# Performance work log

Measured on AMD Instinct MI355X. Metric: run time of the kernel, lower is better.

The kernel has to match this reference:

```python
import jax, jax.numpy as jnp
import numpy as np

B, T, E, H = 4, 2048, 1024, 16
HD = E // H  # head_dim = 64


def setup_inputs() -> dict:
    key = jax.random.key(0)
    ks = jax.random.split(key, 6)
    s_in = 1.0 / np.sqrt(HD)
    s_e = 1.0 / np.sqrt(E)
    return {
        "x": jax.random.normal(ks[0], (B, T, E), dtype=jnp.float32),
        # per-head qkv linear: weight [H, HD, 3*HD], bias [H, 3*HD]
        "W_qkv": jax.random.uniform(ks[1], (H, HD, 3 * HD), dtype=jnp.float32, minval=-s_in, maxval=s_in),
        "b_qkv": jax.random.uniform(ks[2], (H, 3 * HD), dtype=jnp.float32, minval=-s_in, maxval=s_in),
        # output projection [E, E]
        "W_proj": jax.random.uniform(ks[3], (E, E), dtype=jnp.float32, minval=-s_e, maxval=s_e),
        "b_proj": jax.random.uniform(ks[4], (E,), dtype=jnp.float32, minval=-s_e, maxval=s_e),
    }


def reference(x, W_qkv, b_qkv, W_proj, b_proj):
    b, t, e = x.shape
    h, hd = W_qkv.shape[0], W_qkv.shape[1]
    # Each head consumes its own contiguous slice of the channel dim.
    xh = x.reshape(b, t, h, hd)  # [B,T,H,HD]
    qkv = jnp.einsum("bthd,hde->bthe", xh, W_qkv) + b_qkv  # [B,T,H,3*HD]
    q, k, v = jnp.split(qkv, 3, axis=-1)  # each [B,T,H,HD]
    scale = 1.0 / (hd ** 0.5 + 1e-05)  # matches (embed_dim ** 0.5 + 1e-05) with embed_dim=head_dim
    attn = jnp.einsum("bthd,bshd->bhts", q, k) * scale  # [B,H,T,T]
    causal = jnp.tril(jnp.ones((t, t), dtype=bool))
    attn = jnp.where(causal, attn, -jnp.inf)
    attn = jax.nn.softmax(attn, axis=-1)
    out = jnp.einsum("bhts,bshd->bthd", attn, v).reshape(b, t, e)  # concat heads
    # dropout is identity in eval mode
    return out @ W_proj.T + b_proj
```

## Files before the change

### kernel.cpp

```cpp
#include <hip/hip_runtime.h>
#include <hip/hip_bf16.h>

#define B_ 4
#define T_ 2048
#define E_ 1024
#define H_ 16
#define HD_ 64

typedef __attribute__((ext_vector_type(8))) short bf16x8;
typedef __attribute__((ext_vector_type(4))) float f32x4;
typedef __attribute__((ext_vector_type(16))) float f32x16;

__device__ inline ushort f2b(float f) {
  union { __hip_bfloat16 h; ushort u; } c;
  c.h = __float2bfloat16(f);
  return c.u;
}
__device__ inline short f2bs(float f) {
  union { __hip_bfloat16 h; short s; } c;
  c.h = __float2bfloat16(f);
  return c.s;
}
__device__ inline int cvtpk(float lo, float hi) {
  int r;
  asm("v_cvt_pk_bf16_f32 %0, %1, %2" : "=v"(r) : "v"(lo), "v"(hi));
  return r;
}
__device__ inline f32x16 zero16() {
  f32x16 z;
#pragma unroll
  for (int i = 0; i < 16; ++i) z[i] = 0.0f;
  return z;
}

__device__ inline void gload16(const ushort* gsrc, ushort* lds_uniform_base) {
  __builtin_amdgcn_global_load_lds(
      (const __attribute__((address_space(1))) void*)gsrc,
      (__attribute__((address_space(3))) void*)lds_uniform_base, 16, 0, 0);
}

__global__ __launch_bounds__(256) void cvt_w_kernel(const float* __restrict__ Wq,
                                                    ushort* __restrict__ Wt) {
  int gtid = blockIdx.x * 256 + threadIdx.x;
  int h = gtid / (HD_ * 192);
  int rem = gtid % (HD_ * 192);
  int d = rem / 192;
  int e = rem % 192;
  Wt[h * (192 * HD_) + e * HD_ + d] = f2b(Wq[gtid]);
}

__global__ __launch_bounds__(256) void cvt_wproj_kernel(const float* __restrict__ Wp,
                                                        ushort* __restrict__ Wb) {
  int i = (blockIdx.x * 256 + threadIdx.x) * 4;
  float4 f = *reinterpret_cast<const float4*>(Wp + i);
  ushort4 u;
  u.x = f2b(f.x); u.y = f2b(f.y); u.z = f2b(f.z); u.w = f2b(f.w);
  *reinterpret_cast<ushort4*>(Wb + i) = u;
}

__global__ __launch_bounds__(256) void qkv_kernel(const float* __restrict__ x,
                                                  const ushort* __restrict__ Wt,
                                                  const float* __restrict__ bq,
                                                  ushort* __restrict__ Q,
                                                  ushort* __restrict__ K,
                                                  ushort* __restrict__ Vt) {
  const float SCALE = (1.0f / (8.0f + 1e-5f)) * 1.4426950408889634f;
  int wave = threadIdx.x >> 6, lane = threadIdx.x & 63;
  int lo = lane & 15, hi = lane >> 4;
  int bh = blockIdx.y, b = bh >> 4, h = bh & 15;
  int t0 = blockIdx.x * 64 + wave * 16;

  const float* xr = x + (size_t)(b * T_ + t0 + lo) * E_ + h * HD_;
  bf16x8 af[2];
#pragma unroll
  for (int c = 0; c < 2; ++c) {
    float4 f0 = *reinterpret_cast<const float4*>(xr + c * 32 + hi * 8);
    float4 f1 = *reinterpret_cast<const float4*>(xr + c * 32 + hi * 8 + 4);
    bf16x8 v;
    v[0] = f2bs(f0.x); v[1] = f2bs(f0.y); v[2] = f2bs(f0.z); v[3] = f2bs(f0.w);
    v[4] = f2bs(f1.x); v[5] = f2bs(f1.y); v[6] = f2bs(f1.z); v[7] = f2bs(f1.w);
    af[c] = v;
  }

  const ushort* Wh = Wt + h * (192 * HD_);
#pragma unroll
  for (int nt = 0; nt < 12; ++nt) {
    int n0 = nt * 16;
    bf16x8 bf0 = *reinterpret_cast<const bf16x8*>(Wh + (size_t)(n0 + lo) * HD_ + hi * 8);
    bf16x8 bf1 = *reinterpret_cast<const bf16x8*>(Wh + (size_t)(n0 + lo) * HD_ + 32 + hi * 8);
    f32x4 acc = {0.0f, 0.0f, 0.0f, 0.0f};
    acc = __builtin_amdgcn_mfma_f32_16x16x32_bf16(af[0], bf0, acc, 0, 0, 0);
    acc = __builtin_amdgcn_mfma_f32_16x16x32_bf16(af[1], bf1, acc, 0, 0, 0);

    int which = nt >> 2;
    int hd = (nt & 3) * 16 + lo;
    float bias = bq[h * 192 + n0 + lo];
    if (which < 2) {
      ushort* dst = which == 0 ? Q : K;
      float sc = which == 0 ? SCALE : 1.0f;
#pragma unroll
      for (int r = 0; r < 4; ++r) {
        int t = t0 + hi * 4 + r;
        dst[((size_t)bh * T_ + t) * HD_ + hd] = f2b((acc[r] + bias) * sc);
      }
    } else {
      ushort4 u;
      u.x = f2b(acc[0] + bias);
      u.y = f2b(acc[1] + bias);
      u.z = f2b(acc[2] + bias);
      u.w = f2b(acc[3] + bias);
      int col = t0 + hi * 4 + hd * 8;
      col &= (T_ - 1);
      *reinterpret_cast<ushort4*>(Vt + ((size_t)bh * HD_ + hd) * T_ + col) = u;
    }
  }
}

__global__ __launch_bounds__(256) void attn_kernel(const ushort* __restrict__ Q,
                                                   const ushort* __restrict__ K,
                                                   const ushort* __restrict__ Vt,
                                                   ushort* __restrict__ AO) {
  __shared__ ushort Ks[3][64 * 64];
  __shared__ ushort Vs[3][64 * 64];

  int wave = threadIdx.x >> 6, lane = threadIdx.x & 63;
  int q5 = lane & 31, hi5 = lane >> 5;
  int bh = blockIdx.x, b = bh >> 4, h = bh & 15;
  int qt = (T_ / 128 - 1) - blockIdx.y;
  int qw = qt * 128 + wave * 32;

  const ushort* Kbh = K + (size_t)bh * T_ * HD_;
  const ushort* Vbh = Vt + (size_t)bh * HD_ * T_;

  bf16x8 qf[4];
#pragma unroll
  for (int ks = 0; ks < 4; ++ks)
    qf[ks] = *reinterpret_cast<const bf16x8*>(
        Q + ((size_t)bh * T_ + qw + q5) * HD_ + ks * 16 + hi5 * 8);

  f32x16 ot[2];
  ot[0] = zero16(); ot[1] = zero16();
  float mreg = -1e30f, lreg = 0.0f;

  int srow = lane >> 3;
  int sch = lane & 7;

  int ntiles = qt * 2 + 2;

#define STAGE(BUF, TILE)                                                        \
  {                                                                             \
    int kt_ = (TILE) << 6;                                                      \
    _Pragma("unroll")                                                           \
    for (int rep = 0; rep < 2; ++rep) {                                         \
      int row = rep * 32 + wave * 8 + srow;                                     \
      const ushort* gk = Kbh + (size_t)(kt_ + row) * HD_ + ((sch ^ (row & 7)) * 8); \
      gload16(gk, &Ks[BUF][(rep * 32 + wave * 8) * 64]);                        \
      int col = (kt_ + ((sch ^ (row & 7)) + row) * 8) & (T_ - 1);               \
      const ushort* gv = Vbh + (size_t)row * T_ + col;                          \
      gload16(gv, &Vs[BUF][(rep * 32 + wave * 8) * 64]);                        \
    }                                                                           \
  }

  STAGE(0, 0);
  STAGE(1, 1);

  int cur = 0;
  for (int tile = 0; tile < ntiles; ++tile) {
    int kt = tile << 6;
    asm volatile("s_waitcnt vmcnt(4)" ::: "memory");
    __builtin_amdgcn_s_barrier();
    {
      int pre = (tile + 2 < ntiles) ? tile + 2 : 0;
      int pb = cur + 2; if (pb >= 3) pb -= 3;
      STAGE(pb, pre);
    }

    if (kt <= qw + 31) {
      f32x16 s[2];
#pragma unroll
      for (int g = 0; g < 2; ++g) {
        int krow = g * 32 + q5;
        bf16x8 kf[4];
#pragma unroll
        for (int ks = 0; ks < 4; ++ks)
          kf[ks] = *reinterpret_cast<const bf16x8*>(
              &Ks[cur][krow * 64 + (((2 * ks + hi5) ^ (krow & 7)) * 8)]);
        f32x16 acc = zero16();
        __builtin_amdgcn_s_setprio(1);
#pragma unroll
        for (int ks = 0; ks < 4; ++ks)
          acc = __builtin_amdgcn_mfma_f32_32x32x16_bf16(kf[ks], qf[ks], acc, 0, 0, 0);
        __builtin_amdgcn_s_setprio(0);
        s[g] = acc;
      }
      if (kt + 63 > qw) {
        int q = qw + q5;
#pragma unroll
        for (int g = 0; g < 2; ++g)
#pragma unroll
          for (int r = 0; r < 16; ++r) {
            int key = kt + g * 32 + (r & 3) + 8 * (r >> 2) + 4 * hi5;
            if (key > q) s[g][r] = -1e30f;
          }
      }
      float t8[8];
#pragma unroll
      for (int i = 0; i < 8; ++i)
        t8[i] = fmaxf(fmaxf(s[0][i], s[0][i + 8]), fmaxf(s[1][i], s[1][i + 8]));
      float mx = fmaxf(fmaxf(fmaxf(t8[0], t8[1]), fmaxf(t8[2], t8[3])),
                       fmaxf(fmaxf(t8[4], t8[5]), fmaxf(t8[6], t8[7])));
      mx = fmaxf(mx, __shfl_xor(mx, 32));
      float nm = fmaxf(mreg, mx);
      float alpha = exp2f(mreg - nm);
      mreg = nm;
#pragma unroll
      for (int g = 0; g < 2; ++g)
#pragma unroll
        for (int r = 0; r < 16; ++r)
          s[g][r] = exp2f(s[g][r] - nm);
      float u8[8];
#pragma unroll
      for (int i = 0; i < 8; ++i)
        u8[i] = (s[0][i] + s[0][i + 8]) + (s[1][i] + s[1][i + 8]);
      float rs = ((u8[0] + u8[1]) + (u8[2] + u8[3])) + ((u8[4] + u8[5]) + (u8[6] + u8[7]));
      rs += __shfl_xor(rs, 32);
      lreg = lreg * alpha + rs;
#pragma unroll
      for (int nh = 0; nh < 2; ++nh)
#pragma unroll
        for (int r = 0; r < 16; ++r) ot[nh][r] *= alpha;

      bf16x8 pb4[4];
#pragma unroll
      for (int ks = 0; ks < 4; ++ks) {
        int g = ks >> 1;
        int R0 = 2 * (ks & 1), R1 = R0 + 1;
        int a0w0 = cvtpk(s[g][4 * R0 + 0], s[g][4 * R0 + 1]);
        int a0w1 = cvtpk(s[g][4 * R0 + 2], s[g][4 * R0 + 3]);
        int a1w0 = cvtpk(s[g][4 * R1 + 0], s[g][4 * R1 + 1]);
        int a1w1 = cvtpk(s[g][4 * R1 + 2], s[g][4 * R1 + 3]);
        int pA0w0 = __shfl_xor(a0w0, 32);
        int pA0w1 = __shfl_xor(a0w1, 32);
        int pA1w0 = __shfl_xor(a1w0, 32);
        int pA1w1 = __shfl_xor(a1w1, 32);
        int4 w;
        w.x = hi5 ? pA1w0 : a0w0;
        w.y = hi5 ? pA1w1 : a0w1;
        w.z = hi5 ? a1w0 : pA0w0;
        w.w = hi5 ? a1w1 : pA0w1;
        pb4[ks] = *reinterpret_cast<bf16x8*>(&w);
      }
#pragma unroll
      for (int nh = 0; nh < 2; ++nh) {
        int vrow = nh * 32 + q5;
        bf16x8 vf[4];
#pragma unroll
        for (int ks = 0; ks < 4; ++ks)
          vf[ks] = *reinterpret_cast<const bf16x8*>(
              &Vs[cur][vrow * 64 + (((2 * ks + hi5) ^ (vrow & 7)) * 8)]);
        __builtin_amdgcn_s_setprio(1);
#pragma unroll
        for (int ks = 0; ks < 4; ++ks)
          ot[nh] = __builtin_amdgcn_mfma_f32_32x32x16_bf16(vf[ks], pb4[ks], ot[nh], 0, 0, 0);
        __builtin_amdgcn_s_setprio(0);
      }
    }
    cur = (cur == 2) ? 0 : cur + 1;
  }
#undef STAGE

  float inv = 1.0f / lreg;
  int t = qw + q5;
  ushort* aop = AO + ((size_t)(b * T_ + t) * H_ + h) * HD_;
#pragma unroll
  for (int nh = 0; nh < 2; ++nh)
#pragma unroll
    for (int R = 0; R < 4; ++R) {
      ushort4 u;
      u.x = f2b(ot[nh][4 * R + 0] * inv);
      u.y = f2b(ot[nh][4 * R + 1] * inv);
      u.z = f2b(ot[nh][4 * R + 2] * inv);
      u.w = f2b(ot[nh][4 * R + 3] * inv);
      *reinterpret_cast<ushort4*>(aop + nh * 32 + 8 * R + 4 * hi5) = u;
    }
}

__global__ __launch_bounds__(256) void proj_kernel(const ushort* __restrict__ A,
                                                   const ushort* __restrict__ Wb,
                                                   const float* __restrict__ bias,
                                                   float* __restrict__ out) {
  __shared__ ushort As[2][128 * 32];
  __shared__ ushort Bs[2][128 * 32];
  int tid = threadIdx.x;
  int wave = tid >> 6, lane = tid & 63;
  int lo = lane & 15, hi = lane >> 4;
  int wr = wave >> 1, wc = wave & 1;
  int m0 = blockIdx.y * 128, n0 = blockIdx.x * 128;

  int srow4 = lane >> 2;
  int sch4 = lane & 3;
  int swz = sch4 ^ ((srow4 >> 1) & 3);

#define PSTAGE(BUF, K0)                                                          \
  {                                                                              \
    _Pragma("unroll")                                                            \
    for (int rep = 0; rep < 2; ++rep) {                                          \
      int row = wave * 32 + rep * 16 + srow4;                                    \
      gload16(A + (size_t)(m0 + row) * E_ + (K0) + swz * 8,                      \
              &As[BUF][(wave * 32 + rep * 16) * 32]);                            \
      gload16(Wb + (size_t)(n0 + row) * E_ + (K0) + swz * 8,                     \
              &Bs[BUF][(wave * 32 + rep * 16) * 32]);                            \
    }                                                                            \
  }

  f32x4 acc[4][4] = {};
  PSTAGE(0, 0);
  asm volatile("s_waitcnt vmcnt(0)" ::: "memory");
  __syncthreads();

  int cur = 0;
  for (int k0 = 0; k0 < E_; k0 += 32) {
    int kpre = (k0 + 32) & (E_ - 1);
    PSTAGE(cur ^ 1, kpre);
    bf16x8 af[4], bfr[4];
#pragma unroll
    for (int i = 0; i < 4; ++i) {
      int row = wr * 64 + i * 16 + lo;
      af[i] = *reinterpret_cast<const bf16x8*>(
          &As[cur][row * 32 + ((hi ^ ((row >> 1) & 3)) * 8)]);
    }
#pragma unroll
    for (int j = 0; j < 4; ++j) {
      int row = wc * 64 + j * 16 + lo;
      bfr[j] = *reinterpret_cast<const bf16x8*>(
          &Bs[cur][row * 32 + ((hi ^ ((row >> 1) & 3)) * 8)]);
    }
    __builtin_amdgcn_s_setprio(1);
#pragma unroll
    for (int i = 0; i < 4; ++i)
#pragma unroll
      for (int j = 0; j < 4; ++j)
        acc[i][j] = __builtin_amdgcn_mfma_f32_16x16x32_bf16(af[i], bfr[j], acc[i][j], 0, 0, 0);
    __builtin_amdgcn_s_setprio(0);
    asm volatile("s_waitcnt vmcnt(0)" ::: "memory");
    __syncthreads();
    cur ^= 1;
  }
#undef PSTAGE

#pragma unroll
  for (int i = 0; i < 4; ++i)
#pragma unroll
    for (int r = 0; r < 4; ++r) {
      int mm = m0 + wr * 64 + i * 16 + hi * 4 + r;
      float* orow = out + (size_t)mm * E_ + n0 + wc * 64;
#pragma unroll
      for (int j = 0; j < 4; ++j)
        orow[j * 16 + lo] = acc[i][j][r] + bias[n0 + wc * 64 + j * 16 + lo];
    }
}

extern "C" void kernel_launch(void* const* d_in, const int* in_sizes, int n_in,
                              void* d_out, int out_size, void* d_ws, size_t ws_size,
                              hipStream_t stream) {
  (void)in_sizes; (void)n_in; (void)out_size; (void)ws_size;
  const float* x  = (const float*)d_in[0];
  const float* Wq = (const float*)d_in[1];
  const float* bq = (const float*)d_in[2];
  const float* Wp = (const float*)d_in[3];
  const float* bp = (const float*)d_in[4];
  float* out = (float*)d_out;

  const size_t NQ = (size_t)B_ * H_ * T_ * HD_;
  ushort* ws = (ushort*)d_ws;
  ushort* Q  = ws;
  ushort* K  = ws + NQ;
  ushort* Vt = ws + 2 * NQ;
  ushort* AO = ws + 3 * NQ;
  ushort* Wb = ws + 4 * NQ;
  ushort* Wt = ws + 4 * NQ + (size_t)E_ * E_;

  cvt_w_kernel<<<dim3(768), dim3(256), 0, stream>>>(Wq, Wt);
  cvt_wproj_kernel<<<dim3(1024), dim3(256), 0, stream>>>(Wp, Wb);
  qkv_kernel<<<dim3(T_ / 64, B_ * H_), dim3(256), 0, stream>>>(x, Wt, bq, Q, K, Vt);
  attn_kernel<<<dim3(B_ * H_, 16), dim3(256), 0, stream>>>(Q, K, Vt, AO);
  proj_kernel<<<dim3(E_ / 128, (B_ * T_) / 128), dim3(256), 0, stream>>>(AO, Wb, bp, out);
}
```

Baseline: 153.4 us.

## Process two 32-query groups per wave and stage KV tiles in pairs

The attention kernel now gives each wave 64 queries, split into two 32-row groups that share each K/V fragment read from LDS. The block tile grows to 256 queries and the grid shrinks to 8 blocks per head, ordered by interleaving long and short causal rows. Shared memory goes from three to four buffers, and K/V tiles are prefetched two at a time, waiting on all outstanding loads (vmcnt(0)) before each pair. This doubles the MFMA work per LDS read, but raises register pressure, halves the block count, and coarsens load balancing.

Result: slower. 215.2 us (+40.3%).

```diff
diff --git a/kernel.cpp b/kernel.cpp
--- a/kernel.cpp
+++ b/kernel.cpp
@@ -120,32 +120,37 @@
                                                    const ushort* __restrict__ K,
                                                    const ushort* __restrict__ Vt,
                                                    ushort* __restrict__ AO) {
-  __shared__ ushort Ks[3][64 * 64];
-  __shared__ ushort Vs[3][64 * 64];
+  __shared__ ushort Ks[4][64 * 64];
+  __shared__ ushort Vs[4][64 * 64];
 
   int wave = threadIdx.x >> 6, lane = threadIdx.x & 63;
   int q5 = lane & 31, hi5 = lane >> 5;
   int bh = blockIdx.x, b = bh >> 4, h = bh & 15;
-  int qt = (T_ / 128 - 1) - blockIdx.y;
-  int qw = qt * 128 + wave * 32;
+  int y = blockIdx.y;
+  int qt = (y < 4) ? (7 - y) : (y - 4);
+  int qw = qt * 256 + wave * 64;
 
   const ushort* Kbh = K + (size_t)bh * T_ * HD_;
   const ushort* Vbh = Vt + (size_t)bh * HD_ * T_;
 
-  bf16x8 qf[4];
-#pragma unroll
-  for (int ks = 0; ks < 4; ++ks)
-    qf[ks] = *reinterpret_cast<const bf16x8*>(
+  bf16x8 qfA[4], qfB[4];
+#pragma unroll
+  for (int ks = 0; ks < 4; ++ks) {
+    qfA[ks] = *reinterpret_cast<const bf16x8*>(
         Q + ((size_t)bh * T_ + qw + q5) * HD_ + ks * 16 + hi5 * 8);
-
-  f32x16 ot[2];
-  ot[0] = zero16(); ot[1] = zero16();
-  float mreg = -1e30f, lreg = 0.0f;
+    qfB[ks] = *reinterpret_cast<const bf16x8*>(
+        Q + ((size_t)bh * T_ + qw + 32 + q5) * HD_ + ks * 16 + hi5 * 8);
+  }
+
+  f32x16 otA[2], otB[2];
+  otA[0] = zero16(); otA[1] = zero16();
+  otB[0] = zero16(); otB[1] = zero16();
+  float mA = -1e30f, lA = 0.0f, mB = -1e30f, lB = 0.0f;
 
   int srow = lane >> 3;
   int sch = lane & 7;
 
-  int ntiles = qt * 2 + 2;
+  int ntiles = qt * 4 + 4;
 
 #define STAGE(BUF, TILE)                                                        \
   {                                                                             \
@@ -161,128 +166,154 @@
     }                                                                           \
   }
 
+  auto mask_g = [&](f32x16 (&s)[2], int qwg, int kt) {
+    int q = qwg + q5;
+#pragma unroll
+    for (int g = 0; g < 2; ++g)
+#pragma unroll
+      for (int r = 0; r < 16; ++r) {
+        int key = kt + g * 32 + (r & 3) + 8 * (r >> 2) + 4 * hi5;
+        if (key > q) s[g][r] = -1e30f;
+      }
+  };
+  auto softmax_g = [&](f32x16 (&s)[2], float& mreg, float& lreg, f32x16 (&ot)[2]) {
+    float t8[8];
+#pragma unroll
+    for (int i = 0; i < 8; ++i)
+      t8[i] = fmaxf(fmaxf(s[0][i], s[0][i + 8]), fmaxf(s[1][i], s[1][i + 8]));
+    float mx = fmaxf(fmaxf(fmaxf(t8[0], t8[1]), fmaxf(t8[2], t8[3])),
+                     fmaxf(fmaxf(t8[4], t8[5]), fmaxf(t8[6], t8[7])));
+    mx = fmaxf(mx, __shfl_xor(mx, 32));
+    float nm = fmaxf(mreg, mx);
+    float alpha = exp2f(mreg - nm);
+    mreg = nm;
+#pragma unroll
+    for (int g = 0; g < 2; ++g)
+#pragma unroll
+      for (int r = 0; r < 16; ++r)
+        s[g][r] = exp2f(s[g][r] - nm);
+    float u8[8];
+#pragma unroll
+    for (int i = 0; i < 8; ++i)
+      u8[i] = (s[0][i] + s[0][i + 8]) + (s[1][i] + s[1][i + 8]);
+    float rs = ((u8[0] + u8[1]) + (u8[2] + u8[3])) + ((u8[4] + u8[5]) + (u8[6] + u8[7]));
+    rs += __shfl_xor(rs, 32);
+    lreg = lreg * alpha + rs;
+#pragma unroll
+    for (int nh = 0; nh < 2; ++nh)
+#pragma unroll
+      for (int r = 0; r < 16; ++r) ot[nh][r] *= alpha;
+  };
+  auto repack_g = [&](const f32x16 (&s)[2], bf16x8 (&pb)[4]) {
+#pragma unroll
+    for (int ks = 0; ks < 4; ++ks) {
+      int g = ks >> 1;
+      int R0 = 2 * (ks & 1), R1 = R0 + 1;
+      int a0w0 = cvtpk(s[g][4 * R0 + 0], s[g][4 * R0 + 1]);
+      int a0w1 = cvtpk(s[g][4 * R0 + 2], s[g][4 * R0 + 3]);
+      int a1w0 = cvtpk(s[g][4 * R1 + 0], s[g][4 * R1 + 1]);
+      int a1w1 = cvtpk(s[g][4 * R1 + 2], s[g][4 * R1 + 3]);
+      int pA0w0 = __shfl_xor(a0w0, 32);
+      int pA0w1 = __shfl_xor(a0w1, 32);
+      int pA1w0 = __shfl_xor(a1w0, 32);
+      int pA1w1 = __shfl_xor(a1w1, 32);
+      int4 w;
+      w.x = hi5 ? pA1w0 : a0w0;
+      w.y = hi5 ? pA1w1 : a0w1;
+      w.z = hi5 ? a1w0 : pA0w0;
+      w.w = hi5 ? a1w1 : pA0w1;
+      pb[ks] = *reinterpret_cast<bf16x8*>(&w);
+    }
+  };
+
+  auto compute_tile = [&](int tile, int buf) {
+    int kt = tile << 6;
+    if (kt > qw + 31) return;
+    f32x16 sA[2], sB[2];
+#pragma unroll
+    for (int g = 0; g < 2; ++g) {
+      int krow = g * 32 + q5;
+      bf16x8 kf[4];
+#pragma unroll
+      for (int ks = 0; ks < 4; ++ks)
+        kf[ks] = *reinterpret_cast<const bf16x8*>(
+            &Ks[buf][krow * 64 + (((2 * ks + hi5) ^ (krow & 7)) * 8)]);
+      f32x16 aA = zero16(), aB = zero16();
+      __builtin_amdgcn_s_setprio(1);
+#pragma unroll
+      for (int ks = 0; ks < 4; ++ks)
+        aA = __builtin_amdgcn_mfma_f32_32x32x16_bf16(kf[ks], qfA[ks], aA, 0, 0, 0);
+#pragma unroll
+      for (int ks = 0; ks < 4; ++ks)
+        aB = __builtin_amdgcn_mfma_f32_32x32x16_bf16(kf[ks], qfB[ks], aB, 0, 0, 0);
+      __builtin_amdgcn_s_setprio(0);
+      sA[g] = aA; sB[g] = aB;
+    }
+    if (kt + 63 > qw) {
+      mask_g(sA, qw, kt);
+      mask_g(sB, qw + 32, kt);
+    }
+    softmax_g(sA, mA, lA, otA);
+    softmax_g(sB, mB, lB, otB);
+    bf16x8 pbA[4], pbB[4];
+    repack_g(sA, pbA);
+    repack_g(sB, pbB);
+#pragma unroll
+    for (int nh = 0; nh < 2; ++nh) {
+      int vrow = nh * 32 + q5;
+      bf16x8 vf[4];
+#pragma unroll
+      for (int ks = 0; ks < 4; ++ks)
+        vf[ks] = *reinterpret_cast<const bf16x8*>(
+            &Vs[buf][vrow * 64 + (((2 * ks + hi5) ^ (vrow & 7)) * 8)]);
+      __builtin_amdgcn_s_setprio(1);
+#pragma unroll
+      for (int ks = 0; ks < 4; ++ks)
+        otA[nh] = __builtin_amdgcn_mfma_f32_32x32x16_bf16(vf[ks], pbA[ks], otA[nh], 0, 0, 0);
+#pragma unroll
+      for (int ks = 0; ks < 4; ++ks)
+        otB[nh] = __builtin_amdgcn_mfma_f32_32x32x16_bf16(vf[ks], pbB[ks], otB[nh], 0, 0, 0);
+      __builtin_amdgcn_s_setprio(0);
+    }
+  };
+
   STAGE(0, 0);
   STAGE(1, 1);
 
-  int cur = 0;
-  for (int tile = 0; tile < ntiles; ++tile) {
-    int kt = tile << 6;
-    asm volatile("s_waitcnt vmcnt(4)" ::: "memory");
+  int npairs = ntiles >> 1;
+  for (int p = 0; p < npairs; ++p) {
+    int t0 = 2 * p, t1 = 2 * p + 1;
+    asm volatile("s_waitcnt vmcnt(0)" ::: "memory");
     __builtin_amdgcn_s_barrier();
     {
-      int pre = (tile + 2 < ntiles) ? tile + 2 : 0;
-      int pb = cur + 2; if (pb >= 3) pb -= 3;
-      STAGE(pb, pre);
-    }
-
-    if (kt <= qw + 31) {
-      f32x16 s[2];
-#pragma unroll
-      for (int g = 0; g < 2; ++g) {
-        int krow = g * 32 + q5;
-        bf16x8 kf[4];
-#pragma unroll
-        for (int ks = 0; ks < 4; ++ks)
-          kf[ks] = *reinterpret_cast<const bf16x8*>(
-              &Ks[cur][krow * 64 + (((2 * ks + hi5) ^ (krow & 7)) * 8)]);
-        f32x16 acc = zero16();
-        __builtin_amdgcn_s_setprio(1);
-#pragma unroll
-        for (int ks = 0; ks < 4; ++ks)
-          acc = __builtin_amdgcn_mfma_f32_32x32x16_bf16(kf[ks], qf[ks], acc, 0, 0, 0);
-        __builtin_amdgcn_s_setprio(0);
-        s[g] = acc;
+      int pr0 = t0 + 2, pr1 = t0 + 3;
+      int s0 = (pr0 < ntiles) ? pr0 : 0;
+      int s1 = (pr1 < ntiles) ? pr1 : 0;
+      STAGE(pr0 & 3, s0);
+      STAGE(pr1 & 3, s1);
+    }
+    compute_tile(t0, t0 & 3);
+    compute_tile(t1, t1 & 3);
+  }
+#undef STAGE
+
+  auto store_g = [&](const f32x16 (&ot)[2], float lreg, int trow) {
+    float inv = 1.0f / lreg;
+    ushort* aop = AO + ((size_t)(b * T_ + trow) * H_ + h) * HD_;
+#pragma unroll
+    for (int nh = 0; nh < 2; ++nh)
+#pragma unroll
+      for (int R = 0; R < 4; ++R) {
+        ushort4 u;
+        u.x = f2b(ot[nh][4 * R + 0] * inv);
+        u.y = f2b(ot[nh][4 * R + 1] * inv);
+        u.z = f2b(ot[nh][4 * R + 2] * inv);
+        u.w = f2b(ot[nh][4 * R + 3] * inv);
+        *reinterpret_cast<ushort4*>(aop + nh * 32 + 8 * R + 4 * hi5) = u;
       }
-      if (kt + 63 > qw) {
-        int q = qw + q5;
-#pragma unroll
-        for (int g = 0; g < 2; ++g)
-#pragma unroll
-          for (int r = 0; r < 16; ++r) {
-            int key = kt + g * 32 + (r & 3) + 8 * (r >> 2) + 4 * hi5;
-            if (key > q) s[g][r] = -1e30f;
-          }
-      }
-      float t8[8];
-#pragma unroll
-      for (int i = 0; i < 8; ++i)
-        t8[i] = fmaxf(fmaxf(s[0][i], s[0][i + 8]), fmaxf(s[1][i], s[1][i + 8]));
-      float mx = fmaxf(fmaxf(fmaxf(t8[0], t8[1]), fmaxf(t8[2], t8[3])),
-                       fmaxf(fmaxf(t8[4], t8[5]), fmaxf(t8[6], t8[7])));
-      mx = fmaxf(mx, __shfl_xor(mx, 32));
-      float nm = fmaxf(mreg, mx);
-      float alpha = exp2f(mreg - nm);
-      mreg = nm;
-#pragma unroll
-      for (int g = 0; g < 2; ++g)
-#pragma unroll
-        for (int r = 0; r < 16; ++r)
-          s[g][r] = exp2f(s[g][r] - nm);
-      float u8[8];
-#pragma unroll
-      for (int i = 0; i < 8; ++i)
-        u8[i] = (s[0][i] + s[0][i + 8]) + (s[1][i] + s[1][i + 8]);
-      float rs = ((u8[0] + u8[1]) + (u8[2] + u8[3])) + ((u8[4] + u8[5]) + (u8[6] + u8[7]));
-      rs += __shfl_xor(rs, 32);
-      lreg = lreg * alpha + rs;
-#pragma unroll
-      for (int nh = 0; nh < 2; ++nh)
-#pragma unroll
-        for (int r = 0; r < 16; ++r) ot[nh][r] *= alpha;
-
-      bf16x8 pb4[4];
-#pragma unroll
-      for (int ks = 0; ks < 4; ++ks) {
-        int g = ks >> 1;
-        int R0 = 2 * (ks & 1), R1 = R0 + 1;
-        int a0w0 = cvtpk(s[g][4 * R0 + 0], s[g][4 * R0 + 1]);
-        int a0w1 = cvtpk(s[g][4 * R0 + 2], s[g][4 * R0 + 3]);
-        int a1w0 = cvtpk(s[g][4 * R1 + 0], s[g][4 * R1 + 1]);
-        int a1w1 = cvtpk(s[g][4 * R1 + 2], s[g][4 * R1 + 3]);
-        int pA0w0 = __shfl_xor(a0w0, 32);
-        int pA0w1 = __shfl_xor(a0w1, 32);
-        int pA1w0 = __shfl_xor(a1w0, 32);
-        int pA1w1 = __shfl_xor(a1w1, 32);
-        int4 w;
-        w.x = hi5 ? pA1w0 : a0w0;
-        w.y = hi5 ? pA1w1 : a0w1;
-        w.z = hi5 ? a1w0 : pA0w0;
-        w.w = hi5 ? a1w1 : pA0w1;
-        pb4[ks] = *reinterpret_cast<bf16x8*>(&w);
-      }
-#pragma unroll
-      for (int nh = 0; nh < 2; ++nh) {
-        int vrow = nh * 32 + q5;
-        bf16x8 vf[4];
-#pragma unroll
-        for (int ks = 0; ks < 4; ++ks)
-          vf[ks] = *reinterpret_cast<const bf16x8*>(
-              &Vs[cur][vrow * 64 + (((2 * ks + hi5) ^ (vrow & 7)) * 8)]);
-        __builtin_amdgcn_s_setprio(1);
-#pragma unroll
-        for (int ks = 0; ks < 4; ++ks)
-          ot[nh] = __builtin_amdgcn_mfma_f32_32x32x16_bf16(vf[ks], pb4[ks], ot[nh], 0, 0, 0);
-        __builtin_amdgcn_s_setprio(0);
-      }
-    }
-    cur = (cur == 2) ? 0 : cur + 1;
-  }
-#undef STAGE
-
-  float inv = 1.0f / lreg;
-  int t = qw + q5;
-  ushort* aop = AO + ((size_t)(b * T_ + t) * H_ + h) * HD_;
-#pragma unroll
-  for (int nh = 0; nh < 2; ++nh)
-#pragma unroll
-    for (int R = 0; R < 4; ++R) {
-      ushort4 u;
-      u.x = f2b(ot[nh][4 * R + 0] * inv);
-      u.y = f2b(ot[nh][4 * R + 1] * inv);
-      u.z = f2b(ot[nh][4 * R + 2] * inv);
-      u.w = f2b(ot[nh][4 * R + 3] * inv);
-      *reinterpret_cast<ushort4*>(aop + nh * 32 + 8 * R + 4 * hi5) = u;
-    }
+  };
+  store_g(otA, lA, qw + q5);
+  store_g(otB, lB, qw + 32 + q5);
 }
 
 __global__ __launch_bounds__(256) void proj_kernel(const ushort* __restrict__ A,
@@ -383,6 +414,6 @@
   cvt_w_kernel<<<dim3(768), dim3(256), 0, stream>>>(Wq, Wt);
   cvt_wproj_kernel<<<dim3(1024), dim3(256), 0, stream>>>(Wp, Wb);
   qkv_kernel<<<dim3(T_ / 64, B_ * H_), dim3(256), 0, stream>>>(x, Wt, bq, Q, K, Vt);
-  attn_kernel<<<dim3(B_ * H_, 16), dim3(256), 0, stream>>>(Q, K, Vt, AO);
+  attn_kernel<<<dim3(B_ * H_, 8), dim3(256), 0, stream>>>(Q, K, Vt, AO);
   proj_kernel<<<dim3(E_ / 128, (B_ * T_) / 128), dim3(256), 0, stream>>>(AO, Wb, bp, out);
 }
```
